# Optimization experiments

Hardware: AMD Instinct MI355X
Metric: run time of the kernel (lower is better)

Reference implementation:

```python
import jax, jax.numpy as jnp
import numpy as np

B, N, C, H = 2, 2048, 768, 12
HD = C // H
SCALE = HD ** -0.5


def setup_inputs() -> dict:
    key = jax.random.key(0)
    k1, k2, k3, k4 = jax.random.split(key, 4)
    return {
        "x": jax.random.normal(k1, (B, N, C), dtype=jnp.float32),
        "qkv_w": jax.random.normal(k2, (3 * C, C), dtype=jnp.float32) * (C ** -0.5),
        "proj_w": jax.random.normal(k3, (C, C), dtype=jnp.float32) * (C ** -0.5),
        "proj_b": jax.random.normal(k4, (C,), dtype=jnp.float32) * 0.01,
    }


def reference(x, qkv_w, proj_w, proj_b):
    b, n, c = x.shape
    # qkv: Linear(dim, 3*dim, bias=False) -> (B,N,3,H,HD) -> per-tensor (B,H,N,HD)
    qkv = (x @ qkv_w.T).reshape(b, n, 3, H, HD)
    q, k, v = jnp.moveaxis(qkv, 2, 0)          # each (B,N,H,HD)
    q = q.transpose(0, 2, 1, 3)                # (B,H,N,HD)
    k = k.transpose(0, 2, 1, 3)
    v = v.transpose(0, 2, 1, 3)
    attn_logits = jnp.einsum("bhqd,bhkd->bhqk", q, k) * SCALE  # (B,H,N,N)
    attn = jax.nn.softmax(attn_logits, axis=-1)
    score = jnp.mean(attn, axis=1)             # (B,N,N) mean over heads
    # dropout p=0.0 -> identity
    out = jnp.einsum("bhqk,bhkd->bhqd", attn, v)  # (B,H,N,HD)
    out = out.transpose(0, 2, 1, 3).reshape(b, n, c)
    out = out @ proj_w.T + proj_b
    return out, score
```

## Files before the change

### kernel.cpp

```cpp
#include <hip/hip_runtime.h>
#include <cstddef>

typedef __attribute__((ext_vector_type(8))) short bf16x8;
typedef __attribute__((ext_vector_type(4))) float f32x4;
typedef __attribute__((ext_vector_type(16))) float f32x16;

constexpr int Bb = 2, Nn = 2048, Cc = 768, Hh = 12, HDd = 64;
constexpr float QSCALE = 0.125f * 1.44269504088896340736f;

#define VMCNT(n) asm volatile("s_waitcnt vmcnt(" #n ")" ::: "memory")
#define SBAR() __builtin_amdgcn_s_barrier()

__device__ inline short f2bf(float f) {
  unsigned u = __builtin_bit_cast(unsigned, f);
  u += 0x7fff + ((u >> 16) & 1);
  return (short)(u >> 16);
}
__device__ inline unsigned cvtpk(float a, float b) {
  unsigned r;
  asm("v_cvt_pk_bf16_f32 %0, %1, %2" : "=v"(r) : "v"(a), "v"(b));
  return r;
}
__device__ inline void gl_lds16(const void* g, void* l) {
  __builtin_amdgcn_global_load_lds(
      (const __attribute__((address_space(1))) unsigned*)g,
      (__attribute__((address_space(3))) unsigned*)l, 16, 0, 0);
}
__device__ inline bf16x8 lds8(const short* p) { return *(const bf16x8*)p; }
__device__ inline f32x16 zero16() {
  f32x16 z;
#pragma unroll
  for (int r = 0; r < 16; ++r) z[r] = 0.f;
  return z;
}
__device__ inline bf16x8 ld_frag(const short* base, int row, int ch) {
  return *(const bf16x8*)&base[row * 64 + (((ch ^ (row & 7)) << 3))];
}

__global__ __launch_bounds__(256) void cvt3_kernel(
    const float* __restrict__ s0, const float* __restrict__ s1,
    const float* __restrict__ s2, short* __restrict__ d, int n0, int n01) {
  const int i = (blockIdx.x * 256 + threadIdx.x) * 4;
  const float* src;
  int off;
  if (i < n0) {
    src = s0; off = i;
  } else if (i < n01) {
    src = s1; off = i - n0;
  } else {
    src = s2; off = i - n01;
  }
  const float4 v = *(const float4*)&src[off];
  short4 o;
  o.x = f2bf(v.x); o.y = f2bf(v.y); o.z = f2bf(v.z); o.w = f2bf(v.w);
  *(short4*)&d[i] = o;
}

__global__ __launch_bounds__(256) void qkv_mfma(
    const short* __restrict__ A, const short* __restrict__ W,
    short* __restrict__ Qg, short* __restrict__ Kg, short* __restrict__ Vtg) {
  __shared__ short As[2 * 8192];
  __shared__ short Bs[2 * 6144];
  const int t = threadIdx.x, l = t & 63, w = t >> 6;
  const int lr = l & 15, lh = l >> 4;
  const int m0 = blockIdx.x * 128, r0 = blockIdx.y * 96;
  const int wr = w >> 1, wc = w & 1;
  f32x4 acc[4][3];
#pragma unroll
  for (int i = 0; i < 4; ++i)
#pragma unroll
    for (int j = 0; j < 3; ++j) acc[i][j] = (f32x4){0.f, 0.f, 0.f, 0.f};

  auto stage = [&](const int buf, const int kt) {
#pragma unroll
    for (int u = 0; u < 4; ++u) {
      const int cu = u * 4 + w;
      const int du = cu * 64 + l;
      const int row = du >> 3, ch = du & 7, sch = ch ^ (row & 7);
      gl_lds16(A + (size_t)(m0 + row) * Cc + kt * 64 + sch * 8,
               &As[buf * 8192 + cu * 512]);
    }
#pragma unroll
    for (int u = 0; u < 3; ++u) {
      const int cu = u * 4 + w;
      const int du = cu * 64 + l;
      const int row = du >> 3, ch = du & 7, sch = ch ^ (row & 7);
      gl_lds16(W + (size_t)(r0 + row) * Cc + kt * 64 + sch * 8,
               &Bs[buf * 6144 + cu * 512]);
    }
  };
  auto compute = [&](const int buf) {
    const short* Ab = As + buf * 8192;
    const short* Bbp = Bs + buf * 6144;
#pragma unroll
    for (int kp = 0; kp < 2; ++kp) {
      bf16x8 af[4], bfv[3];
#pragma unroll
      for (int i = 0; i < 4; ++i)
        af[i] = ld_frag(Ab, wr * 64 + i * 16 + lr, kp * 4 + lh);
#pragma unroll
      for (int j = 0; j < 3; ++j)
        bfv[j] = ld_frag(Bbp, wc * 48 + j * 16 + lr, kp * 4 + lh);
      __builtin_amdgcn_s_setprio(1);
#pragma unroll
      for (int i = 0; i < 4; ++i)
#pragma unroll
        for (int j = 0; j < 3; ++j)
          acc[i][j] = __builtin_amdgcn_mfma_f32_16x16x32_bf16(
              af[i], bfv[j], acc[i][j], 0, 0, 0);
      __builtin_amdgcn_s_setprio(0);
    }
  };

  stage(0, 0);
#pragma unroll 1
  for (int kk = 0; kk < 10; kk += 2) {
    stage(1, kk + 1);
    VMCNT(7); SBAR();
    compute(0);
    SBAR();
    stage(0, kk + 2);
    VMCNT(7); SBAR();
    compute(1);
    SBAR();
  }
  stage(1, 11);
  VMCNT(7); SBAR();
  compute(0);
  SBAR();
  VMCNT(0); SBAR();
  compute(1);

  const int which = r0 / Cc;
  const int rbase = r0 % Cc;
  const int bq = m0 >> 11;
  const int nb = (m0 & 2047) + wr * 64;
  if (which == 2) {
#pragma unroll
    for (int j = 0; j < 3; ++j) {
      const int rr = rbase + wc * 48 + j * 16 + lr;
      const int head = rr >> 6, dd = rr & 63;
      short* vp = &Vtg[(((size_t)bq * Hh + head) * HDd + dd) * Nn];
#pragma unroll
      for (int i = 0; i < 4; ++i) {
        short4 o;
        o.x = f2bf(acc[i][j][0]); o.y = f2bf(acc[i][j][1]);
        o.z = f2bf(acc[i][j][2]); o.w = f2bf(acc[i][j][3]);
        *(short4*)&vp[nb + i * 16 + lh * 4] = o;
      }
    }
  } else {
    const float scl = (which == 0) ? QSCALE : 1.0f;
    short* __restrict__ dst = (which == 0) ? Qg : Kg;
#pragma unroll
    for (int j = 0; j < 3; ++j) {
      const int rr = rbase + wc * 48 + j * 16 + lr;
      const int head = rr >> 6, dd = rr & 63;
      short* dp = &dst[((size_t)bq * Hh + head) * Nn * HDd + dd];
#pragma unroll
      for (int i = 0; i < 4; ++i)
#pragma unroll
        for (int r = 0; r < 4; ++r)
          dp[(size_t)(nb + i * 16 + lh * 4 + r) * HDd] =
              f2bf(acc[i][j][r] * scl);
    }
  }
}

__global__ __launch_bounds__(256, 3) void attn_pass1(
    const short* __restrict__ Qg, const short* __restrict__ Kg,
    const short* __restrict__ Vtg, float* __restrict__ Linv,
    short* __restrict__ OHb) {
  __shared__ short SM[4 * 4096 + 4 * 1024];
  const int t = threadIdx.x, l = t & 63, w = t >> 6;
  const int lr = l & 15, lh = l >> 4;
  const int raw = blockIdx.x;
  const int bid = (raw & 7) * 96 + (raw >> 3);
  const int q0 = (bid & 31) * 64;
  const int head = (bid >> 5) % Hh;
  const int b = bid / (32 * Hh);
  const size_t base = (size_t)b * Hh + head;
  const short* Qh = Qg + base * Nn * HDd;
  const short* Kh = Kg + base * Nn * HDd;
  const short* Vh = Vtg + base * HDd * Nn;
  const int qw = q0 + w * 16;
  const int PB = 16384 + w * 1024;

  const bf16x8 onesf = {0x3F80, 0x3F80, 0x3F80, 0x3F80,
                        0x3F80, 0x3F80, 0x3F80, 0x3F80};

  int fof[2][4], wofi[4], pof[2];
#pragma unroll
  for (int kp = 0; kp < 2; ++kp) {
#pragma unroll
    for (int i = 0; i < 4; ++i)
      fof[kp][i] = (i * 16 + lr) * 64 + (((kp * 4 + lh) ^ (lr & 7)) << 3);
    pof[kp] = lr * 64 + (((kp * 4 + lh) ^ (lr & 7)) << 3);
  }
#pragma unroll
  for (int i = 0; i < 4; ++i) {
    const int ch = 2 * i + (lh >> 1);
    wofi[i] = lr * 64 + ((ch ^ (lr & 7)) << 3) + (lh & 1) * 4;
  }

  bf16x8 qf[2];
#pragma unroll
  for (int kp = 0; kp < 2; ++kp)
    qf[kp] = *(const bf16x8*)&Qh[(size_t)(qw + lr) * HDd + kp * 32 + lh * 8];

  f32x4 accO[4], accL;
  accL = (f32x4){0.f, 0.f, 0.f, 0.f};
#pragma unroll
  for (int j = 0; j < 4; ++j) accO[j] = (f32x4){0.f, 0.f, 0.f, 0.f};

  auto stage = [&](const int buf, const int tile) {
    const short* Kt = Kh + (size_t)tile * (64 * HDd);
    const short* Vt = Vh + tile * 64;
#pragma unroll
    for (int u = 0; u < 2; ++u) {
      const int cu = u * 4 + w;
      const int du = cu * 64 + l;
      const int row = du >> 3, ch = du & 7, sch = ch ^ (row & 7);
      gl_lds16(Kt + row * 64 + sch * 8, &SM[buf * 4096 + cu * 512]);
      gl_lds16(Vt + (size_t)row * Nn + sch * 8,
               &SM[8192 + buf * 4096 + cu * 512]);
    }
  };

  auto compute = [&](const int kb) {
    const int vb = 8192 + kb;
    f32x4 sacc[4];
#pragma unroll
    for (int i = 0; i < 4; ++i) sacc[i] = (f32x4){0.f, 0.f, 0.f, 0.f};
    __builtin_amdgcn_s_setprio(1);
#pragma unroll
    for (int kp = 0; kp < 2; ++kp)
#pragma unroll
      for (int i = 0; i < 4; ++i)
        sacc[i] = __builtin_amdgcn_mfma_f32_16x16x32_bf16(
            lds8(&SM[kb + fof[kp][i]]), qf[kp], sacc[i], 0, 0, 0);
    __builtin_amdgcn_s_setprio(0);
#pragma unroll
    for (int i = 0; i < 4; ++i) {
      const float p0 = exp2f(sacc[i][0]), p1 = exp2f(sacc[i][1]);
      const float p2 = exp2f(sacc[i][2]), p3 = exp2f(sacc[i][3]);
      uint2 pk;
      pk.x = cvtpk(p0, p1);
      pk.y = cvtpk(p2, p3);
      *(uint2*)&SM[PB + wofi[i]] = pk;
    }
    __builtin_amdgcn_s_setprio(1);
#pragma unroll
    for (int kp = 0; kp < 2; ++kp) {
      const bf16x8 pa = lds8(&SM[PB + pof[kp]]);
      accL = __builtin_amdgcn_mfma_f32_16x16x32_bf16(pa, onesf, accL, 0, 0, 0);
#pragma unroll
      for (int j = 0; j < 4; ++j)
        accO[j] = __builtin_amdgcn_mfma_f32_16x16x32_bf16(
            pa, lds8(&SM[vb + fof[kp][j]]), accO[j], 0, 0, 0);
    }
    __builtin_amdgcn_s_setprio(0);
  };

  stage(0, 0);
#pragma unroll 1
  for (int it = 0; it < 30; it += 2) {
    stage(1, it + 1);
    VMCNT(4); SBAR();
    compute(0);
    SBAR();
    stage(0, it + 2);
    VMCNT(4); SBAR();
    compute(4096);
    SBAR();
  }
  stage(1, 31);
  VMCNT(4); SBAR();
  compute(0);
  SBAR();
  VMCNT(0); SBAR();
  compute(4096);

  f32x4 linvq;
#pragma unroll
  for (int r = 0; r < 4; ++r) linvq[r] = 1.0f / accL[r];
  if (lr == 0) *(f32x4*)&Linv[base * Nn + qw + 4 * lh] = linvq;
#pragma unroll
  for (int j = 0; j < 4; ++j)
#pragma unroll
    for (int r = 0; r < 4; ++r)
      OHb[((size_t)b * Nn + qw + 4 * lh + r) * Cc + head * HDd + j * 16 + lr] =
          f2bf(accO[j][r] * linvq[r]);
}

__global__ __launch_bounds__(256, 4) void score_mfma(
    const short* __restrict__ Qg, const short* __restrict__ Kg,
    const float* __restrict__ Linv, float* __restrict__ score) {
  __shared__ __align__(16) char SMraw[128 * 66 * 4];
  short* SK = (short*)SMraw;
  float* SOUT = (float*)SMraw;
  const int t = threadIdx.x, l = t & 63, w = t >> 6;
  const int lo5 = l & 31, hi5 = l >> 5;
  const int raw = blockIdx.x;
  const int xcd = raw & 7, idx = raw >> 3;
  const int b = xcd >> 2;
  const int q0 = ((xcd & 3) * 4 + (idx >> 5)) * 128;
  const int kv0 = (idx & 31) * 64;
  const int qw = q0 + w * 32;

  int of2[2][4];
#pragma unroll
  for (int i = 0; i < 2; ++i)
#pragma unroll
    for (int s = 0; s < 4; ++s)
      of2[i][s] = (i * 32 + lo5) * 64 + ((((2 * s + hi5) ^ (l & 7))) << 3);

  f32x16 sc0 = zero16(), sc1 = zero16();

  auto stage = [&](const int kb, const int h) {
    const short* Kt = Kg + (((size_t)b * Hh + h) * Nn + kv0) * HDd;
#pragma unroll
    for (int u = 0; u < 2; ++u) {
      const int cu = u * 4 + w;
      const int du = cu * 64 + l;
      const int row = du >> 3, ch = du & 7, sch = ch ^ (row & 7);
      gl_lds16(Kt + row * 64 + sch * 8, &SK[kb + cu * 512]);
    }
  };

  stage(0, 0);
  __syncthreads();
#pragma unroll 1
  for (int h = 0; h < Hh; ++h) {
    if (h + 1 < Hh) stage(((h + 1) & 1) * 4096, h + 1);
    const size_t hb = (size_t)b * Hh + h;
    bf16x8 qf0 = *(const bf16x8*)&Qg[(hb * Nn + qw + lo5) * HDd + 0 + hi5 * 8];
    bf16x8 qf1 = *(const bf16x8*)&Qg[(hb * Nn + qw + lo5) * HDd + 16 + hi5 * 8];
    bf16x8 qf2 = *(const bf16x8*)&Qg[(hb * Nn + qw + lo5) * HDd + 32 + hi5 * 8];
    bf16x8 qf3 = *(const bf16x8*)&Qg[(hb * Nn + qw + lo5) * HDd + 48 + hi5 * 8];
    const float lv = Linv[hb * Nn + qw + lo5];
    const int kb = (h & 1) * 4096;
    f32x16 s0 = zero16(), s1 = zero16();
    __builtin_amdgcn_s_setprio(1);
    s0 = __builtin_amdgcn_mfma_f32_32x32x16_bf16(lds8(&SK[kb + of2[0][0]]),
                                                 qf0, s0, 0, 0, 0);
    s1 = __builtin_amdgcn_mfma_f32_32x32x16_bf16(lds8(&SK[kb + of2[1][0]]),
                                                 qf0, s1, 0, 0, 0);
    s0 = __builtin_amdgcn_mfma_f32_32x32x16_bf16(lds8(&SK[kb + of2[0][1]]),
                                                 qf1, s0, 0, 0, 0);
    s1 = __builtin_amdgcn_mfma_f32_32x32x16_bf16(lds8(&SK[kb + of2[1][1]]),
                                                 qf1, s1, 0, 0, 0);
    s0 = __builtin_amdgcn_mfma_f32_32x32x16_bf16(lds8(&SK[kb + of2[0][2]]),
                                                 qf2, s0, 0, 0, 0);
    s1 = __builtin_amdgcn_mfma_f32_32x32x16_bf16(lds8(&SK[kb + of2[1][2]]),
                                                 qf2, s1, 0, 0, 0);
    s0 = __builtin_amdgcn_mfma_f32_32x32x16_bf16(lds8(&SK[kb + of2[0][3]]),
                                                 qf3, s0, 0, 0, 0);
    s1 = __builtin_amdgcn_mfma_f32_32x32x16_bf16(lds8(&SK[kb + of2[1][3]]),
                                                 qf3, s1, 0, 0, 0);
    __builtin_amdgcn_s_setprio(0);
#pragma unroll
    for (int r = 0; r < 16; ++r) {
      sc0[r] += exp2f(s0[r]) * lv;
      sc1[r] += exp2f(s1[r]) * lv;
    }
    __syncthreads();
  }

  constexpr float invH = 1.0f / 12.0f;
  const int qrow = (w * 32 + lo5) * 66;
#pragma unroll
  for (int g = 0; g < 4; ++g) {
    f32x4 o0, o1;
#pragma unroll
    for (int e = 0; e < 4; ++e) {
      o0[e] = sc0[4 * g + e] * invH;
      o1[e] = sc1[4 * g + e] * invH;
    }
    *(f32x4*)&SOUT[qrow + 8 * g + 4 * hi5] = o0;
    *(f32x4*)&SOUT[qrow + 32 + 8 * g + 4 * hi5] = o1;
  }
  __syncthreads();
#pragma unroll
  for (int s = 0; s < 8; ++s) {
    const int unit = s * 256 + t;
    const int row = unit >> 4, c = unit & 15;
    const f32x4 v = *(const f32x4*)&SOUT[row * 66 + c * 4];
    *(f32x4*)&score[((size_t)b * Nn + q0 + row) * Nn + kv0 + c * 4] = v;
  }
}

__global__ __launch_bounds__(256) void proj_mfma(
    const short* __restrict__ A, const short* __restrict__ W,
    const float* __restrict__ bias, float* __restrict__ out) {
  __shared__ short As[2 * 4096];
  __shared__ short Bs[2 * 4096];
  const int t = threadIdx.x, l = t & 63, w = t >> 6;
  const int lr = l & 15, lh = l >> 4;
  const int m0 = blockIdx.x * 64, c0 = blockIdx.y * 64;
  const int wr = w >> 1, wc = w & 1;
  f32x4 acc[2][2];
#pragma unroll
  for (int i = 0; i < 2; ++i)
#pragma unroll
    for (int j = 0; j < 2; ++j) acc[i][j] = (f32x4){0.f, 0.f, 0.f, 0.f};

  auto stage = [&](const int buf, const int kt) {
#pragma unroll
    for (int u = 0; u < 2; ++u) {
      const int cu = u * 4 + w;
      const int du = cu * 64 + l;
      const int row = du >> 3, ch = du & 7, sch = ch ^ (row & 7);
      gl_lds16(A + (size_t)(m0 + row) * Cc + kt * 64 + sch * 8,
               &As[buf * 4096 + cu * 512]);
      gl_lds16(W + (size_t)(c0 + row) * Cc + kt * 64 + sch * 8,
               &Bs[buf * 4096 + cu * 512]);
    }
  };
  auto compute = [&](const int buf) {
    const short* Ab = As + buf * 4096;
    const short* Bbp = Bs + buf * 4096;
#pragma unroll
    for (int kp = 0; kp < 2; ++kp) {
      bf16x8 af[2], bfv[2];
#pragma unroll
      for (int i = 0; i < 2; ++i)
        af[i] = ld_frag(Ab, wr * 32 + i * 16 + lr, kp * 4 + lh);
#pragma unroll
      for (int j = 0; j < 2; ++j)
        bfv[j] = ld_frag(Bbp, wc * 32 + j * 16 + lr, kp * 4 + lh);
      __builtin_amdgcn_s_setprio(1);
#pragma unroll
      for (int i = 0; i < 2; ++i)
#pragma unroll
        for (int j = 0; j < 2; ++j)
          acc[i][j] = __builtin_amdgcn_mfma_f32_16x16x32_bf16(
              af[i], bfv[j], acc[i][j], 0, 0, 0);
      __builtin_amdgcn_s_setprio(0);
    }
  };

  stage(0, 0);
#pragma unroll 1
  for (int kk = 0; kk < 10; kk += 2) {
    stage(1, kk + 1);
    VMCNT(4); SBAR();
    compute(0);
    SBAR();
    stage(0, kk + 2);
    VMCNT(4); SBAR();
    compute(1);
    SBAR();
  }
  stage(1, 11);
  VMCNT(4); SBAR();
  compute(0);
  SBAR();
  VMCNT(0); SBAR();
  compute(1);

#pragma unroll
  for (int j = 0; j < 2; ++j) {
    const int c = c0 + wc * 32 + j * 16 + lr;
    const float bi = bias[c];
#pragma unroll
    for (int i = 0; i < 2; ++i)
#pragma unroll
      for (int r = 0; r < 4; ++r) {
        const int m = m0 + wr * 32 + i * 16 + lh * 4 + r;
        out[(size_t)m * Cc + c] = acc[i][j][r] + bi;
      }
  }
}

extern "C" void kernel_launch(void* const* d_in, const int* in_sizes, int n_in,
                              void* d_out, int out_size, void* d_ws,
                              size_t ws_size, hipStream_t stream) {
  const float* x = (const float*)d_in[0];
  const float* qkv_w = (const float*)d_in[1];
  const float* proj_w = (const float*)d_in[2];
  const float* proj_b = (const float*)d_in[3];

  float* out = (float*)d_out;
  float* score = out + (size_t)Bb * Nn * Cc;

  const size_t nx = (size_t)Bb * Nn * Cc;
  const size_t nwq = (size_t)3 * Cc * Cc;
  const size_t npw = (size_t)Cc * Cc;
  short* xb = (short*)d_ws;
  short* wqb = xb + nx;
  short* pwb = wqb + nwq;
  short* Qb = pwb + npw;
  short* Kb = Qb + nx;
  short* Vtb = Kb + nx;
  short* OHb = Vtb + nx;
  float* Linv = (float*)(OHb + nx);

  const int ncvt = (int)((nx + nwq + npw) / 1024);
  cvt3_kernel<<<dim3(ncvt), 256, 0, stream>>>(x, qkv_w, proj_w, xb, (int)nx,
                                              (int)(nx + nwq));
  qkv_mfma<<<dim3(32, 24), 256, 0, stream>>>(xb, wqb, Qb, Kb, Vtb);
  attn_pass1<<<dim3(768), 256, 0, stream>>>(Qb, Kb, Vtb, Linv, OHb);
  score_mfma<<<dim3(1024), 256, 0, stream>>>(Qb, Kb, Linv, score);
  proj_mfma<<<dim3(64, 12), 256, 0, stream>>>(OHb, pwb, proj_b, out);
}
```

Baseline: 129.2 us.

## Software-pipeline score kernel head loop to overlap exp with next head's MFMA

Restructures the per-head loop in score_mfma into a two-stage software pipeline. Q fragments for the next head are prefetched into registers, and the exp2/accumulate of one head runs alongside the QK MFMAs of the following head. The goal is to hide global Q load latency and to overlap transcendental work with matrix ops. Holding twice the fragment and score registers raises register pressure, so launch bounds drop from 4 to 3 blocks per SM, which lowers occupancy.

```diff
diff --git a/kernel.cpp b/kernel.cpp
--- a/kernel.cpp
+++ b/kernel.cpp
@@ -293,7 +293,7 @@
           f2bf(accO[j][r] * linvq[r]);
 }
 
-__global__ __launch_bounds__(256, 4) void score_mfma(
+__global__ __launch_bounds__(256, 3) void score_mfma(
     const short* __restrict__ Qg, const short* __restrict__ Kg,
     const float* __restrict__ Linv, float* __restrict__ score) {
   __shared__ __align__(16) char SMraw[128 * 66 * 4];
@@ -327,45 +327,76 @@
       gl_lds16(Kt + row * 64 + sch * 8, &SK[kb + cu * 512]);
     }
   };
-
-  stage(0, 0);
-  __syncthreads();
-#pragma unroll 1
-  for (int h = 0; h < Hh; ++h) {
-    if (h + 1 < Hh) stage(((h + 1) & 1) * 4096, h + 1);
-    const size_t hb = (size_t)b * Hh + h;
-    bf16x8 qf0 = *(const bf16x8*)&Qg[(hb * Nn + qw + lo5) * HDd + 0 + hi5 * 8];
-    bf16x8 qf1 = *(const bf16x8*)&Qg[(hb * Nn + qw + lo5) * HDd + 16 + hi5 * 8];
-    bf16x8 qf2 = *(const bf16x8*)&Qg[(hb * Nn + qw + lo5) * HDd + 32 + hi5 * 8];
-    bf16x8 qf3 = *(const bf16x8*)&Qg[(hb * Nn + qw + lo5) * HDd + 48 + hi5 * 8];
-    const float lv = Linv[hb * Nn + qw + lo5];
-    const int kb = (h & 1) * 4096;
-    f32x16 s0 = zero16(), s1 = zero16();
+  auto ldq = [&](const int h, bf16x8& f0, bf16x8& f1, bf16x8& f2,
+                 bf16x8& f3) {
+    const short* Qh = Qg + ((size_t)b * Hh + h) * Nn * HDd;
+    f0 = *(const bf16x8*)&Qh[(size_t)(qw + lo5) * HDd + 0 + hi5 * 8];
+    f1 = *(const bf16x8*)&Qh[(size_t)(qw + lo5) * HDd + 16 + hi5 * 8];
+    f2 = *(const bf16x8*)&Qh[(size_t)(qw + lo5) * HDd + 32 + hi5 * 8];
+    f3 = *(const bf16x8*)&Qh[(size_t)(qw + lo5) * HDd + 48 + hi5 * 8];
+  };
+  auto qk = [&](const int kb, const bf16x8 f0, const bf16x8 f1,
+                const bf16x8 f2, const bf16x8 f3, f32x16& s0, f32x16& s1) {
+    s0 = zero16();
+    s1 = zero16();
     __builtin_amdgcn_s_setprio(1);
     s0 = __builtin_amdgcn_mfma_f32_32x32x16_bf16(lds8(&SK[kb + of2[0][0]]),
-                                                 qf0, s0, 0, 0, 0);
+                                                 f0, s0, 0, 0, 0);
     s1 = __builtin_amdgcn_mfma_f32_32x32x16_bf16(lds8(&SK[kb + of2[1][0]]),
-                                                 qf0, s1, 0, 0, 0);
+                                                 f0, s1, 0, 0, 0);
     s0 = __builtin_amdgcn_mfma_f32_32x32x16_bf16(lds8(&SK[kb + of2[0][1]]),
-                                                 qf1, s0, 0, 0, 0);
+                                                 f1, s0, 0, 0, 0);
     s1 = __builtin_amdgcn_mfma_f32_32x32x16_bf16(lds8(&SK[kb + of2[1][1]]),
-                                                 qf1, s1, 0, 0, 0);
+                                                 f1, s1, 0, 0, 0);
     s0 = __builtin_amdgcn_mfma_f32_32x32x16_bf16(lds8(&SK[kb + of2[0][2]]),
-                                                 qf2, s0, 0, 0, 0);
+                                                 f2, s0, 0, 0, 0);
     s1 = __builtin_amdgcn_mfma_f32_32x32x16_bf16(lds8(&SK[kb + of2[1][2]]),
-                                                 qf2, s1, 0, 0, 0);
+                                                 f2, s1, 0, 0, 0);
     s0 = __builtin_amdgcn_mfma_f32_32x32x16_bf16(lds8(&SK[kb + of2[0][3]]),
-                                                 qf3, s0, 0, 0, 0);
+                                                 f3, s0, 0, 0, 0);
     s1 = __builtin_amdgcn_mfma_f32_32x32x16_bf16(lds8(&SK[kb + of2[1][3]]),
-                                                 qf3, s1, 0, 0, 0);
+                                                 f3, s1, 0, 0, 0);
     __builtin_amdgcn_s_setprio(0);
+  };
+  auto expacc = [&](const f32x16& s0, const f32x16& s1, const float lv) {
 #pragma unroll
     for (int r = 0; r < 16; ++r) {
       sc0[r] += exp2f(s0[r]) * lv;
       sc1[r] += exp2f(s1[r]) * lv;
     }
+  };
+
+  bf16x8 qA0, qA1, qA2, qA3, qB0, qB1, qB2, qB3;
+  f32x16 sA0, sA1, sB0, sB1;
+  float lvA, lvB;
+  stage(0, 0);
+  ldq(0, qA0, qA1, qA2, qA3);
+  __syncthreads();
+  stage(4096, 1);
+  ldq(1, qB0, qB1, qB2, qB3);
+  lvA = Linv[((size_t)b * Hh + 0) * Nn + qw + lo5];
+  qk(0, qA0, qA1, qA2, qA3, sA0, sA1);
+  __syncthreads();
+#pragma unroll 1
+  for (int h = 1; h < 11; h += 2) {
+    stage(0, h + 1);
+    ldq(h + 1, qA0, qA1, qA2, qA3);
+    lvB = Linv[((size_t)b * Hh + h) * Nn + qw + lo5];
+    qk(4096, qB0, qB1, qB2, qB3, sB0, sB1);
+    expacc(sA0, sA1, lvA);
     __syncthreads();
-  }
+    stage(4096, h + 2);
+    ldq(h + 2, qB0, qB1, qB2, qB3);
+    lvA = Linv[((size_t)b * Hh + h + 1) * Nn + qw + lo5];
+    qk(0, qA0, qA1, qA2, qA3, sA0, sA1);
+    expacc(sB0, sB1, lvB);
+    __syncthreads();
+  }
+  lvB = Linv[((size_t)b * Hh + 11) * Nn + qw + lo5];
+  qk(4096, qB0, qB1, qB2, qB3, sB0, sB1);
+  expacc(sA0, sA1, lvA);
+  expacc(sB0, sB1, lvB);
+  __syncthreads();
 
   constexpr float invH = 1.0f / 12.0f;
   const int qrow = (w * 32 + lo5) * 66;
```

New measurement: 154.6 us. 1.2x slower.
